# Optimization experiments

Hardware: AMD Instinct MI355X
Metric: run time of the kernel (lower is better)

The kernel has to match this reference:

```python
import jax, jax.numpy as jnp
import numpy as np
import math

N, E, C, H = 16384, 8192, 256, 8
NNZ = 262144  # incidence pairs, avg vertex degree 16


def setup_inputs() -> dict:
    key = jax.random.key(0)
    ks = jax.random.split(key, 12)
    s = 1.0 / math.sqrt(C)
    inp = {
        "X": jax.random.normal(ks[0], (N, C), dtype=jnp.float32),
        "v_ids": jax.random.randint(ks[1], (NNZ,), 0, N, dtype=jnp.int32),
        "e_ids": jax.random.randint(ks[2], (NNZ,), 0, E, dtype=jnp.int32),
        # Linear params stored as [in, out]; y = x @ W + b  (matches torch x @ W.T + b)
        "Wq": jax.random.uniform(ks[3], (C, C), jnp.float32, -s, s),
        "bq": jax.random.uniform(ks[4], (C,), jnp.float32, -s, s),
        "Wk": jax.random.uniform(ks[5], (C, C), jnp.float32, -s, s),
        "bk": jax.random.uniform(ks[6], (C,), jnp.float32, -s, s),
        "Wv": jax.random.uniform(ks[7], (C, C), jnp.float32, -s, s),
        "bv": jax.random.uniform(ks[8], (C,), jnp.float32, -s, s),
        "Wke": jax.random.uniform(ks[9], (C, C), jnp.float32, -s, s),
        "bke": jax.random.uniform(ks[10], (C,), jnp.float32, -s, s),
    }
    return inp


def reference(X, v_ids, e_ids, Wq, bq, Wk, bk, Wv, bv, Wke, bke):
    d = C // H
    scale = 1.0 / math.sqrt(d)

    Q = (X @ Wq + bq).reshape(N, H, d)
    K = (X @ Wk + bk).reshape(N, H, d)
    V = (X @ Wv + bv).reshape(N, H, d)

    # hg.v2e_aggregation(X, 'mean'): segment-mean of incident vertex features per hyperedge
    sums = jax.ops.segment_sum(X[v_ids], e_ids, num_segments=E)          # [E, C]
    cnt = jax.ops.segment_sum(jnp.ones((NNZ,), X.dtype), e_ids, num_segments=E)
    Xe = sums / jnp.maximum(cnt, 1.0)[:, None]                            # [E, C]

    Ke = Xe @ Wke + bke                                                   # [E, C]
    Qe = X @ Wq + bq                                                      # [N, C]

    # per-node attention over heads: [N, H, H]
    attn_n = jax.nn.softmax(jnp.einsum('nhd,ngd->nhg', Q, K) * scale, axis=-1)
    X_node = jnp.einsum('nhg,ngd->nhd', attn_n, V).reshape(N, C)          # [N, C]

    # node -> hyperedge attention: [N, E]
    attn_e = jax.nn.softmax((Qe @ Ke.T) * scale, axis=-1)
    X_hyperedge = attn_e @ Xe                                             # [N, C]

    out = X_node + X_hyperedge
    # is_last=False: ReLU; bn=None; dropout in eval mode (identity)
    return jax.nn.relu(out)
```

## Files before the change

### kernel.cpp

```cpp
#include <hip/hip_runtime.h>

typedef unsigned short u16;
typedef unsigned int u32;
typedef __attribute__((ext_vector_type(4))) float f32x4;
typedef __attribute__((ext_vector_type(16))) float f32x16;
typedef __attribute__((ext_vector_type(8))) short bf16x8;
typedef __attribute__((ext_vector_type(4))) short bf16x4;
typedef __attribute__((ext_vector_type(4))) u16 u16x4;

#define N_NODES 16384
#define N_EDGES 8192
#define FK_SCALE 0.17677669529663687f
#define LOG2E 1.4426950408889634f
#define C1EXP (FK_SCALE * LOG2E)

typedef const u32 __attribute__((address_space(1))) gu32;
typedef u32 __attribute__((address_space(3))) lu32;

__device__ __forceinline__ void gl_lds16(const void* g, void* l) {
  __builtin_amdgcn_global_load_lds((gu32*)g, (lu32*)l, 16, 0, 0);
}

__device__ __forceinline__ float b2f(u16 u) {
  return __builtin_bit_cast(float, (u32)u << 16);
}
__device__ __forceinline__ u16 f2b(float f) {
  u32 u = __builtin_bit_cast(u32, f);
  u += 0x7fffu + ((u >> 16) & 1u);
  return (u16)(u >> 16);
}

__global__ __launch_bounds__(256) void k_prep(const float* __restrict__ X,
                                              const int* __restrict__ e_ids,
                                              u16* __restrict__ Xb,
                                              int* __restrict__ hist) {
  int i = blockIdx.x * 256 + threadIdx.x;
  f32x4 v = *(const f32x4*)(X + i * 4);
  u16x4 r;
  r.x = f2b(v.x); r.y = f2b(v.y); r.z = f2b(v.z); r.w = f2b(v.w);
  *(u16x4*)(Xb + i * 4) = r;
  if (threadIdx.x < 64) atomicAdd(&hist[e_ids[blockIdx.x * 64 + threadIdx.x]], 1);
}

__global__ __launch_bounds__(256) void k_wt(const float* __restrict__ Wq,
                                            const float* __restrict__ Wk,
                                            const float* __restrict__ Wv,
                                            const float* __restrict__ Wke,
                                            const float* __restrict__ bq,
                                            const float* __restrict__ bk,
                                            const float* __restrict__ bv,
                                            const float* __restrict__ bke,
                                            u16* __restrict__ Wt,
                                            float* __restrict__ bcat) {
  __shared__ float tile[64][65];
  int w = blockIdx.z;
  const float* W = (w == 0) ? Wq : (w == 1) ? Wk : (w == 2) ? Wv : Wke;
  int k0 = blockIdx.x * 64, n0 = blockIdx.y * 64;
  int tid = threadIdx.x;
  if (blockIdx.x == 0 && blockIdx.y == 0) {
    const float* b = (w == 0) ? bq : (w == 1) ? bk : (w == 2) ? bv : bke;
    bcat[w * 256 + tid] = b[tid];
  }
#pragma unroll
  for (int i = 0; i < 16; i++) {
    int idx = i * 256 + tid;
    int kr = idx >> 6, nc = idx & 63;
    tile[nc][kr] = W[(k0 + kr) * 256 + n0 + nc];
  }
  __syncthreads();
#pragma unroll
  for (int i = 0; i < 16; i++) {
    int idx = i * 256 + tid;
    int nr = idx >> 6, kc = idx & 63;
    Wt[w * 65536 + (n0 + nr) * 256 + k0 + kc] = f2b(tile[nr][kc]);
  }
}

__global__ __launch_bounds__(256) void k_scan(const int* __restrict__ hist,
                                              int* __restrict__ eoff,
                                              int* __restrict__ cur) {
  __shared__ int ts[256];
  int t = threadIdx.x;
  int base = t * 32;
  int vals[32];
  int s = 0;
#pragma unroll
  for (int i = 0; i < 32; i++) { vals[i] = hist[base + i]; s += vals[i]; }
  ts[t] = s;
  __syncthreads();
  for (int off = 1; off < 256; off <<= 1) {
    int v = (t >= off) ? ts[t - off] : 0;
    __syncthreads();
    ts[t] += v;
    __syncthreads();
  }
  int ex = ts[t] - s;
#pragma unroll
  for (int i = 0; i < 32; i++) {
    eoff[base + i] = ex;
    cur[base + i] = ex;
    ex += vals[i];
  }
  if (t == 255) eoff[8192] = ex;
}

__global__ __launch_bounds__(256) void k_perm(const int* __restrict__ v_ids,
                                              const int* __restrict__ e_ids,
                                              int* __restrict__ cur,
                                              int* __restrict__ perm) {
  int base = blockIdx.x * 1024 + threadIdx.x;
#pragma unroll
  for (int k = 0; k < 4; k++) {
    int i = base + k * 256;
    int e = e_ids[i];
    int v = v_ids[i];
    int pos = atomicAdd(&cur[e], 1);
    perm[pos] = v;
  }
}

__global__ __launch_bounds__(256) void k_gather(const u16* __restrict__ Xb,
                                                const int* __restrict__ perm,
                                                const int* __restrict__ eoff,
                                                u16* __restrict__ Xe,
                                                u16* __restrict__ XeTc) {
  __shared__ float red[4][256];
  int e = blockIdx.x;
  int tid = threadIdx.x, wave = tid >> 6, lane = tid & 63;
  int start = eoff[e], end = eoff[e + 1];
  f32x4 acc = {0.f, 0.f, 0.f, 0.f};
  for (int j = start + wave; j < end; j += 4) {
    int v = perm[j];
    bf16x4 x = *(const bf16x4*)(Xb + v * 256 + lane * 4);
#pragma unroll
    for (int c = 0; c < 4; c++) acc[c] += b2f((u16)x[c]);
  }
  *(f32x4*)&red[wave][lane * 4] = acc;
  __syncthreads();
  int t = tid;
  float s = red[0][t] + red[1][t] + red[2][t] + red[3][t];
  float m = s / fmaxf((float)(end - start), 1.0f);
  u16 b = f2b(m);
  Xe[e * 256 + t] = b;
  XeTc[(size_t)(e >> 3) * 2048 + t * 8 + (e & 7)] = b;
}

__global__ __launch_bounds__(256) void k_gemm128(const u16* __restrict__ A,
                                                 const u16* __restrict__ Wt,
                                                 const float* __restrict__ bias,
                                                 u16* __restrict__ out,
                                                 int ldout, int tmode) {
  __shared__ u16 As[128 * 64];
  __shared__ u16 Bs[128 * 64];
  int tid = threadIdx.x;
  int wave = tid >> 6, lane = tid & 63;
  int quad = lane >> 4, l16 = lane & 15;
  int wm = wave >> 1, wn = wave & 1;
  int mtile = blockIdx.x * 128, ntile = blockIdx.y * 128;
  const u16* Ap = A + (size_t)mtile * 256;
  const u16* Bp = Wt + (size_t)ntile * 256;

  f32x4 acc[4][4];
#pragma unroll
  for (int am = 0; am < 4; am++)
#pragma unroll
    for (int bn = 0; bn < 4; bn++) acc[am][bn] = (f32x4){0.f, 0.f, 0.f, 0.f};

  for (int ks = 0; ks < 4; ks++) {
    __syncthreads();
#pragma unroll
    for (int i = 0; i < 4; i++) {
      int s = i * 256 + tid;
      int r = s >> 3, c = s & 7;
      gl_lds16(Ap + r * 256 + ks * 64 + ((c ^ (r & 7)) << 3), As + s * 8);
    }
#pragma unroll
    for (int i = 0; i < 4; i++) {
      int s = i * 256 + tid;
      int r = s >> 3, c = s & 7;
      gl_lds16(Bp + r * 256 + ks * 64 + ((c ^ (r & 7)) << 3), Bs + s * 8);
    }
    __syncthreads();
#pragma unroll
    for (int kc = 0; kc < 2; kc++) {
      bf16x8 a[4], b[4];
      int cc = kc * 4 + quad;
#pragma unroll
      for (int am = 0; am < 4; am++) {
        int rl = wm * 64 + am * 16 + l16;
        a[am] = *(const bf16x8*)(As + rl * 64 + ((cc ^ (rl & 7)) << 3));
      }
#pragma unroll
      for (int bn = 0; bn < 4; bn++) {
        int rl = wn * 64 + bn * 16 + l16;
        b[bn] = *(const bf16x8*)(Bs + rl * 64 + ((cc ^ (rl & 7)) << 3));
      }
#pragma unroll
      for (int am = 0; am < 4; am++)
#pragma unroll
        for (int bn = 0; bn < 4; bn++)
          acc[am][bn] = __builtin_amdgcn_mfma_f32_16x16x32_bf16(a[am], b[bn], acc[am][bn], 0, 0, 0);
    }
  }
#pragma unroll
  for (int am = 0; am < 4; am++)
#pragma unroll
    for (int bn = 0; bn < 4; bn++)
#pragma unroll
      for (int r = 0; r < 4; r++) {
        int row = mtile + wm * 64 + am * 16 + quad * 4 + r;
        int col = ntile + wn * 64 + bn * 16 + l16;
        u16 v = f2b(acc[am][bn][r] + bias[col]);
        if (tmode == 0) out[(size_t)row * ldout + col] = v;
        else out[(size_t)(col >> 3) * 65536 + row * 8 + (col & 7)] = v;
      }
}

__global__ __launch_bounds__(256, 2) void k_flash(const u16* __restrict__ QKV,
                                                  const u16* __restrict__ KebT,
                                                  const u16* __restrict__ XeTc,
                                                  u16* __restrict__ Op,
                                                  float* __restrict__ Lv) {
  extern __shared__ u16 sm[];
  u16* KeL = sm;
  u16* VLT = sm + 16384;
  u16* PL = sm + 32768;
  int tid = threadIdx.x;
  int wave = tid >> 6, lane = tid & 63;
  int l31 = lane & 31, half = lane >> 5;
  int pair = wave >> 1, kh = wave & 1;
  int qt = blockIdx.x & 255;
  int split = blockIdx.x >> 8;
  int rowp0 = qt * 64 + pair * 32;
  u16* PLp = PL + pair * 2048;

  bf16x8 qf[16];
#pragma unroll
  for (int ks = 0; ks < 16; ks++)
    qf[ks] = *(const bf16x8*)(QKV + (rowp0 + l31) * 768 + ks * 16 + half * 8);

  f32x16 o[4];
#pragma unroll
  for (int i = 0; i < 4; i++)
#pragma unroll
    for (int r = 0; r < 16; r++) o[i][r] = 0.f;
  float l[16];
#pragma unroll
  for (int r = 0; r < 16; r++) l[r] = 0.f;

  for (int ktl = 0; ktl < 64; ktl++) {
    int ktg = split * 64 + ktl;
    int kbase = ktg * 64;
    __syncthreads();
#pragma unroll
    for (int i = 0; i < 8; i++) {
      int s = i * 256 + tid;
      int c = s >> 6, r = s & 63;
      gl_lds16(KebT + ((size_t)c * 8192 + kbase + r) * 8, KeL + s * 8);
    }
    int kb8 = ktg * 8;
#pragma unroll
    for (int i = 0; i < 8; i++) {
      int s = i * 256 + tid;
      int kc = s >> 8, ch = s & 255;
      gl_lds16(XeTc + ((size_t)(kb8 + kc) * 256 + ch) * 8, VLT + s * 8);
    }
    __syncthreads();

    f32x16 sc;
#pragma unroll
    for (int r = 0; r < 16; r++) sc[r] = 0.f;
#pragma unroll
    for (int ks = 0; ks < 16; ks++) {
      int c = ks * 2 + half;
      bf16x8 kb = *(const bf16x8*)(KeL + c * 512 + (kh * 32 + l31) * 8);
      sc = __builtin_amdgcn_mfma_f32_32x32x16_bf16(qf[ks], kb, sc, 0, 0, 0);
    }
#pragma unroll
    for (int reg = 0; reg < 16; reg++) {
      float pv = __builtin_amdgcn_exp2f(sc[reg] * C1EXP);
      l[reg] += pv;
      int row = (reg & 3) + 8 * (reg >> 2) + 4 * half;
      int col = kh * 32 + l31;
      PLp[row * 64 + (((col >> 3) ^ (row & 7)) << 3) + (col & 7)] = f2b(pv);
    }
    __syncthreads();
    bf16x8 pf[4];
#pragma unroll
    for (int ks = 0; ks < 4; ks++) {
      int pc = ks * 2 + half;
      pf[ks] = *(const bf16x8*)(PLp + l31 * 64 + ((pc ^ (l31 & 7)) << 3));
    }
#pragma unroll
    for (int ct = 0; ct < 4; ct++) {
#pragma unroll
      for (int ks = 0; ks < 4; ks++) {
        int kc = ks * 2 + half;
        int ch = kh * 128 + ct * 32 + l31;
        bf16x8 vb = *(const bf16x8*)(VLT + kc * 2048 + ch * 8);
        o[ct] = __builtin_amdgcn_mfma_f32_32x32x16_bf16(pf[ks], vb, o[ct], 0, 0, 0);
      }
    }
  }

#pragma unroll
  for (int off = 1; off < 32; off <<= 1)
#pragma unroll
    for (int r = 0; r < 16; r++) l[r] += __shfl_xor(l[r], off, 64);
  if (l31 == 0) {
#pragma unroll
    for (int reg = 0; reg < 16; reg++) {
      int row = (reg & 3) + 8 * (reg >> 2) + 4 * half;
      Lv[(split * 2 + kh) * N_NODES + rowp0 + row] = l[reg];
    }
  }

  size_t obase = (size_t)split * N_NODES * 256;
#pragma unroll
  for (int ct = 0; ct < 4; ct++)
#pragma unroll
    for (int reg = 0; reg < 16; reg++) {
      int row = rowp0 + (reg & 3) + 8 * (reg >> 2) + 4 * half;
      int col = kh * 128 + ct * 32 + l31;
      Op[obase + (size_t)row * 256 + col] = f2b(o[ct][reg]);
    }
}

__global__ __launch_bounds__(256) void k_comb(const u16* __restrict__ QKV,
                                              const u16* __restrict__ Op,
                                              const float* __restrict__ Lv,
                                              float* __restrict__ out) {
  int idx = blockIdx.x * 256 + threadIdx.x;
  int n = idx >> 6, lane = idx & 63;
  int h = lane >> 3, g = lane & 7;
  const u16* base = QKV + n * 768;
  const bf16x8* qp = (const bf16x8*)(base + h * 32);
  const bf16x8* kp = (const bf16x8*)(base + 256 + g * 32);
  float s = 0.f;
#pragma unroll
  for (int t = 0; t < 4; t++) {
    bf16x8 qv = qp[t], kv = kp[t];
#pragma unroll
    for (int j = 0; j < 8; j++) s += b2f((u16)qv[j]) * b2f((u16)kv[j]);
  }
  s *= FK_SCALE;
  float mx = s;
#pragma unroll
  for (int off = 1; off < 8; off <<= 1) mx = fmaxf(mx, __shfl_xor(mx, off, 64));
  float p = __builtin_amdgcn_exp2f((s - mx) * LOG2E);
  float lsum = p;
#pragma unroll
  for (int off = 1; off < 8; off <<= 1) lsum += __shfl_xor(lsum, off, 64);
  float attn = p / lsum;
  float a4[4] = {0.f, 0.f, 0.f, 0.f};
#pragma unroll
  for (int g2 = 0; g2 < 8; g2++) {
    float a = __shfl(attn, (lane & 56) | g2, 64);
    bf16x4 vv = *(const bf16x4*)(base + 512 + g2 * 32 + g * 4);
#pragma unroll
    for (int j = 0; j < 4; j++) a4[j] += a * b2f((u16)vv[j]);
  }
  int c4 = lane * 4;
  float L = 0.f;
#pragma unroll
  for (int sl = 0; sl < 4; sl++) L += Lv[sl * N_NODES + n];
  f32x4 acc = {0.f, 0.f, 0.f, 0.f};
#pragma unroll
  for (int sp = 0; sp < 2; sp++) {
    u16x4 ov = *(const u16x4*)(Op + (size_t)sp * N_NODES * 256 + (size_t)n * 256 + c4);
    acc.x += b2f(ov.x);
    acc.y += b2f(ov.y);
    acc.z += b2f(ov.z);
    acc.w += b2f(ov.w);
  }
  float invL = 1.0f / L;
  f32x4 res;
  res.x = fmaxf(acc.x * invL + a4[0], 0.f);
  res.y = fmaxf(acc.y * invL + a4[1], 0.f);
  res.z = fmaxf(acc.z * invL + a4[2], 0.f);
  res.w = fmaxf(acc.w * invL + a4[3], 0.f);
  *(f32x4*)(out + (size_t)n * 256 + c4) = res;
}

extern "C" void kernel_launch(void* const* d_in, const int* in_sizes, int n_in,
                              void* d_out, int out_size, void* d_ws, size_t ws_size,
                              hipStream_t stream) {
  const float* X = (const float*)d_in[0];
  const int* v_ids = (const int*)d_in[1];
  const int* e_ids = (const int*)d_in[2];
  const float* Wq = (const float*)d_in[3];
  const float* bq = (const float*)d_in[4];
  const float* Wk = (const float*)d_in[5];
  const float* bk = (const float*)d_in[6];
  const float* Wv = (const float*)d_in[7];
  const float* bv = (const float*)d_in[8];
  const float* Wke = (const float*)d_in[9];
  const float* bke = (const float*)d_in[10];
  float* out = (float*)d_out;

  char* ws = (char*)d_ws;
  u16* Xb = (u16*)(ws);
  u16* QKV = (u16*)(ws + 8388608);
  u16* Wt = (u16*)(ws + 33554432);
  float* bcat = (float*)(ws + 34078720);
  int* hist = (int*)(ws + 34082816);
  int* eoff = (int*)(ws + 34115584);
  int* cur = (int*)(ws + 34152448);
  int* perm = (int*)(ws + 34185216);
  u16* Xe = (u16*)(ws + 35233792);
  u16* XeTc = (u16*)(ws + 39428096);
  u16* KebT = (u16*)(ws + 43622400);
  u16* Op = (u16*)(ws + 64593920);
  float* Lv = (float*)(ws + 98148352);

  hipMemsetAsync(hist, 0, 32768, stream);
  k_prep<<<4096, 256, 0, stream>>>(X, e_ids, Xb, hist);
  k_wt<<<dim3(4, 4, 4), 256, 0, stream>>>(Wq, Wk, Wv, Wke, bq, bk, bv, bke, Wt, bcat);
  k_scan<<<1, 256, 0, stream>>>(hist, eoff, cur);
  k_perm<<<256, 256, 0, stream>>>(v_ids, e_ids, cur, perm);
  k_gather<<<8192, 256, 0, stream>>>(Xb, perm, eoff, Xe, XeTc);
  k_gemm128<<<dim3(128, 6), 256, 0, stream>>>(Xb, Wt, bcat, QKV, 768, 0);
  k_gemm128<<<dim3(64, 2), 256, 0, stream>>>(Xe, Wt + 3 * 65536, bcat + 768, KebT, 0, 1);
  hipFuncSetAttribute((const void*)k_flash, hipFuncAttributeMaxDynamicSharedMemorySize,
                      73728);
  k_flash<<<512, 256, 73728, stream>>>(QKV, KebT, XeTc, Op, Lv);
  k_comb<<<4096, 256, 0, stream>>>(QKV, Op, Lv, out);
}
```

Before: 366.8 us.

## Merge prep and weight-transpose kernels, one wave per hyperedge gather, split score MFMA chains

```diff
diff --git a/kernel.cpp b/kernel.cpp
--- a/kernel.cpp
+++ b/kernel.cpp
@@ -33,33 +33,36 @@
 __global__ __launch_bounds__(256) void k_prep(const float* __restrict__ X,
                                               const int* __restrict__ e_ids,
                                               u16* __restrict__ Xb,
-                                              int* __restrict__ hist) {
-  int i = blockIdx.x * 256 + threadIdx.x;
-  f32x4 v = *(const f32x4*)(X + i * 4);
-  u16x4 r;
-  r.x = f2b(v.x); r.y = f2b(v.y); r.z = f2b(v.z); r.w = f2b(v.w);
-  *(u16x4*)(Xb + i * 4) = r;
-  if (threadIdx.x < 64) atomicAdd(&hist[e_ids[blockIdx.x * 64 + threadIdx.x]], 1);
-}
-
-__global__ __launch_bounds__(256) void k_wt(const float* __restrict__ Wq,
-                                            const float* __restrict__ Wk,
-                                            const float* __restrict__ Wv,
-                                            const float* __restrict__ Wke,
-                                            const float* __restrict__ bq,
-                                            const float* __restrict__ bk,
-                                            const float* __restrict__ bv,
-                                            const float* __restrict__ bke,
-                                            u16* __restrict__ Wt,
-                                            float* __restrict__ bcat) {
+                                              int* __restrict__ hist,
+                                              const float* __restrict__ Wq,
+                                              const float* __restrict__ Wk,
+                                              const float* __restrict__ Wv,
+                                              const float* __restrict__ Wke,
+                                              const float* __restrict__ bq,
+                                              const float* __restrict__ bk,
+                                              const float* __restrict__ bv,
+                                              const float* __restrict__ bke,
+                                              u16* __restrict__ Wt,
+                                              float* __restrict__ bcat) {
   __shared__ float tile[64][65];
-  int w = blockIdx.z;
+  int b = blockIdx.x;
+  int tid = threadIdx.x;
+  if (b < 4096) {
+    int i = b * 256 + tid;
+    f32x4 v = *(const f32x4*)(X + (size_t)i * 4);
+    u16x4 r;
+    r.x = f2b(v.x); r.y = f2b(v.y); r.z = f2b(v.z); r.w = f2b(v.w);
+    *(u16x4*)(Xb + (size_t)i * 4) = r;
+    if (tid < 64) atomicAdd(&hist[e_ids[b * 64 + tid]], 1);
+    return;
+  }
+  int local = b - 4096;
+  int w = local >> 4, rem = local & 15;
+  int k0 = (rem >> 2) * 64, n0 = (rem & 3) * 64;
   const float* W = (w == 0) ? Wq : (w == 1) ? Wk : (w == 2) ? Wv : Wke;
-  int k0 = blockIdx.x * 64, n0 = blockIdx.y * 64;
-  int tid = threadIdx.x;
-  if (blockIdx.x == 0 && blockIdx.y == 0) {
-    const float* b = (w == 0) ? bq : (w == 1) ? bk : (w == 2) ? bv : bke;
-    bcat[w * 256 + tid] = b[tid];
+  if (rem == 0) {
+    const float* bb = (w == 0) ? bq : (w == 1) ? bk : (w == 2) ? bv : bke;
+    bcat[w * 256 + tid] = bb[tid];
   }
 #pragma unroll
   for (int i = 0; i < 16; i++) {
@@ -124,25 +127,26 @@
                                                 const int* __restrict__ eoff,
                                                 u16* __restrict__ Xe,
                                                 u16* __restrict__ XeTc) {
-  __shared__ float red[4][256];
-  int e = blockIdx.x;
   int tid = threadIdx.x, wave = tid >> 6, lane = tid & 63;
+  int e = blockIdx.x * 4 + wave;
   int start = eoff[e], end = eoff[e + 1];
   f32x4 acc = {0.f, 0.f, 0.f, 0.f};
-  for (int j = start + wave; j < end; j += 4) {
+  for (int j = start; j < end; j++) {
     int v = perm[j];
-    bf16x4 x = *(const bf16x4*)(Xb + v * 256 + lane * 4);
+    bf16x4 x = *(const bf16x4*)(Xb + (size_t)v * 256 + lane * 4);
 #pragma unroll
     for (int c = 0; c < 4; c++) acc[c] += b2f((u16)x[c]);
   }
-  *(f32x4*)&red[wave][lane * 4] = acc;
-  __syncthreads();
-  int t = tid;
-  float s = red[0][t] + red[1][t] + red[2][t] + red[3][t];
-  float m = s / fmaxf((float)(end - start), 1.0f);
-  u16 b = f2b(m);
-  Xe[e * 256 + t] = b;
-  XeTc[(size_t)(e >> 3) * 2048 + t * 8 + (e & 7)] = b;
+  float inv = 1.0f / fmaxf((float)(end - start), 1.0f);
+  u16x4 r;
+  r.x = f2b(acc.x * inv); r.y = f2b(acc.y * inv);
+  r.z = f2b(acc.z * inv); r.w = f2b(acc.w * inv);
+  *(u16x4*)(Xe + (size_t)e * 256 + lane * 4) = r;
+  size_t tb = (size_t)(e >> 3) * 2048 + (e & 7);
+  XeTc[tb + (lane * 4 + 0) * 8] = r.x;
+  XeTc[tb + (lane * 4 + 1) * 8] = r.y;
+  XeTc[tb + (lane * 4 + 2) * 8] = r.z;
+  XeTc[tb + (lane * 4 + 3) * 8] = r.w;
 }
 
 __global__ __launch_bounds__(256) void k_gemm128(const u16* __restrict__ A,
@@ -267,18 +271,21 @@
     }
     __syncthreads();
 
-    f32x16 sc;
-#pragma unroll
-    for (int r = 0; r < 16; r++) sc[r] = 0.f;
-#pragma unroll
-    for (int ks = 0; ks < 16; ks++) {
-      int c = ks * 2 + half;
-      bf16x8 kb = *(const bf16x8*)(KeL + c * 512 + (kh * 32 + l31) * 8);
-      sc = __builtin_amdgcn_mfma_f32_32x32x16_bf16(qf[ks], kb, sc, 0, 0, 0);
+    f32x16 sc0, sc1;
+#pragma unroll
+    for (int r = 0; r < 16; r++) { sc0[r] = 0.f; sc1[r] = 0.f; }
+#pragma unroll
+    for (int ks = 0; ks < 8; ks++) {
+      int c0 = ks * 2 + half;
+      int c1 = (ks + 8) * 2 + half;
+      bf16x8 kb0 = *(const bf16x8*)(KeL + c0 * 512 + (kh * 32 + l31) * 8);
+      bf16x8 kb1 = *(const bf16x8*)(KeL + c1 * 512 + (kh * 32 + l31) * 8);
+      sc0 = __builtin_amdgcn_mfma_f32_32x32x16_bf16(qf[ks], kb0, sc0, 0, 0, 0);
+      sc1 = __builtin_amdgcn_mfma_f32_32x32x16_bf16(qf[ks + 8], kb1, sc1, 0, 0, 0);
     }
 #pragma unroll
     for (int reg = 0; reg < 16; reg++) {
-      float pv = __builtin_amdgcn_exp2f(sc[reg] * C1EXP);
+      float pv = __builtin_amdgcn_exp2f((sc0[reg] + sc1[reg]) * C1EXP);
       l[reg] += pv;
       int row = (reg & 3) + 8 * (reg >> 2) + 4 * half;
       int col = kh * 32 + l31;
@@ -414,11 +421,11 @@
   float* Lv = (float*)(ws + 98148352);
 
   hipMemsetAsync(hist, 0, 32768, stream);
-  k_prep<<<4096, 256, 0, stream>>>(X, e_ids, Xb, hist);
-  k_wt<<<dim3(4, 4, 4), 256, 0, stream>>>(Wq, Wk, Wv, Wke, bq, bk, bv, bke, Wt, bcat);
+  k_prep<<<4160, 256, 0, stream>>>(X, e_ids, Xb, hist, Wq, Wk, Wv, Wke,
+                                   bq, bk, bv, bke, Wt, bcat);
   k_scan<<<1, 256, 0, stream>>>(hist, eoff, cur);
   k_perm<<<256, 256, 0, stream>>>(v_ids, e_ids, cur, perm);
-  k_gather<<<8192, 256, 0, stream>>>(Xb, perm, eoff, Xe, XeTc);
+  k_gather<<<2048, 256, 0, stream>>>(Xb, perm, eoff, Xe, XeTc);
   k_gemm128<<<dim3(128, 6), 256, 0, stream>>>(Xb, Wt, bcat, QKV, 768, 0);
   k_gemm128<<<dim3(64, 2), 256, 0, stream>>>(Xe, Wt + 3 * 65536, bcat + 768, KebT, 0, 1);
   hipFuncSetAttribute((const void*)k_flash, hipFuncAttributeMaxDynamicSharedMemorySize,
```

After: 350.8 us. 4.4% less time.
